# Kernel optimization log

Hardware: AMD Instinct MI355X
Metric: run time of the kernel (lower is better)

Reference implementation:

```python
import jax, jax.numpy as jnp
import numpy as np

B, S, E, H, D = 2, 2048, 1024, 16, 64  # batch, seq(=max_seq_len), embed_dim, heads, atten_dim


def setup_inputs() -> dict:
    key = jax.random.key(0)
    ks = jax.random.split(key, 9)
    s = 0.02
    return {
        "x": jax.random.normal(ks[0], (B, S, E), jnp.float32),
        "Wq": jax.random.normal(ks[1], (H, E, D), jnp.float32) * s,
        "Wk": jax.random.normal(ks[2], (H, E, D), jnp.float32) * s,
        "Wv": jax.random.normal(ks[3], (H, E, D), jnp.float32) * s,
        "bq": jax.random.normal(ks[4], (H, D), jnp.float32) * s,
        "bk": jax.random.normal(ks[5], (H, D), jnp.float32) * s,
        "bv": jax.random.normal(ks[6], (H, D), jnp.float32) * s,
        "Wp": jax.random.normal(ks[7], (H * D, E), jnp.float32) * s,
        "bp": jax.random.normal(ks[8], (E,), jnp.float32) * s,
    }


def reference(x, Wq, Wk, Wv, bq, bk, bv, Wp, bp):
    scale = jnp.sqrt(jnp.float32(D))
    # per-head projections, all heads at once: [B,H,S,D]
    q = jnp.einsum("bse,hed->bhsd", x, Wq) + bq[:, None, :]
    k = jnp.einsum("bse,hed->bhsd", x, Wk) + bk[:, None, :]
    v = jnp.einsum("bse,hed->bhsd", x, Wv) + bv[:, None, :]
    # causal scores [B,H,S,S], additive -inf mask above diagonal (as in the buffer)
    score = jnp.einsum("bhsd,bhtd->bhst", q, k) / scale
    mask = jnp.triu(jnp.full((S, S), -jnp.inf, jnp.float32), k=1)
    score = score + mask
    probs = jax.nn.softmax(score, axis=-1)
    attn = jnp.einsum("bhst,bhtd->bhsd", probs, v)
    # concat heads -> [B,S,H*D], then projection + ReLU
    concat = attn.transpose(0, 2, 1, 3).reshape(B, S, H * D)
    out = jax.nn.relu(concat @ Wp + bp)
    return out
```

## Files before the change

### kernel.cpp

```cpp
#include <hip/hip_runtime.h>

#define S_LEN 2048
#define E_DIM 1024
#define H_NUM 16
#define D_DIM 64

typedef unsigned short u16;
using bf16x8 = __attribute__((ext_vector_type(8))) short;
using f32x4  = __attribute__((ext_vector_type(4))) float;

#define MFMA16(A, B, C) __builtin_amdgcn_mfma_f32_16x16x32_bf16(A, B, C, 0, 0, 0)

__device__ __forceinline__ u16 f2bf(float f) {
    unsigned u = __float_as_uint(f);
    u += 0x7fffu + ((u >> 16) & 1u);
    return (u16)(u >> 16);
}
__device__ __forceinline__ f32x4 fzero4() { f32x4 z; z[0]=0.f; z[1]=0.f; z[2]=0.f; z[3]=0.f; return z; }

__device__ __forceinline__ void gll16(const u16* g, u16* l) {
    __builtin_amdgcn_global_load_lds(
        (const __attribute__((address_space(1))) void*)g,
        (__attribute__((address_space(3))) void*)l, 16, 0, 0);
}

__global__ __launch_bounds__(256) void cvt_bf16(const float* __restrict__ in, u16* __restrict__ outp, int n) {
    int i4 = (blockIdx.x * 256 + threadIdx.x) * 4;
    if (i4 < n) {
        float4 f = *(const float4*)(in + i4);
        unsigned lo = (unsigned)f2bf(f.x) | ((unsigned)f2bf(f.y) << 16);
        unsigned hi = (unsigned)f2bf(f.z) | ((unsigned)f2bf(f.w) << 16);
        uint2 p; p.x = lo; p.y = hi;
        *(uint2*)(outp + i4) = p;
    }
}

__device__ __forceinline__ void cvt_t_tile(const float* __restrict__ bin, u16* __restrict__ bout,
                                           int R, int C, int r0, int c0) {
    __shared__ float t[64][65];
    const int tid = threadIdx.x;
    const int lr = tid >> 2, lc = (tid & 3) * 16;

    const float* src = bin + (size_t)(r0 + lr) * C + c0 + lc;
    #pragma unroll
    for (int j = 0; j < 4; j++) {
        float4 f = *(const float4*)(src + j * 4);
        t[lr][lc + j * 4 + 0] = f.x; t[lr][lc + j * 4 + 1] = f.y;
        t[lr][lc + j * 4 + 2] = f.z; t[lr][lc + j * 4 + 3] = f.w;
    }
    __syncthreads();

    u16* dst = bout + (size_t)(c0 + lr) * R + r0 + lc;
    u16 vals[16];
    #pragma unroll
    for (int i = 0; i < 16; i++) vals[i] = f2bf(t[lc + i][lr]);
    uint4 pa, pb;
    pa.x = vals[0] | (vals[1] << 16);  pa.y = vals[2] | (vals[3] << 16);
    pa.z = vals[4] | (vals[5] << 16);  pa.w = vals[6] | (vals[7] << 16);
    pb.x = vals[8] | (vals[9] << 16);  pb.y = vals[10] | (vals[11] << 16);
    pb.z = vals[12] | (vals[13] << 16); pb.w = vals[14] | (vals[15] << 16);
    *(uint4*)dst = pa;
    *(uint4*)(dst + 8) = pb;
}

__global__ __launch_bounds__(256) void cvt_bf16_t(const float* __restrict__ in, u16* __restrict__ outp,
                                                  int R, int C) {
    const float* bin = in + (size_t)blockIdx.z * R * C;
    u16* bout = outp + (size_t)blockIdx.z * R * C;
    cvt_t_tile(bin, bout, R, C, blockIdx.y * 64, blockIdx.x * 64);
}

__global__ __launch_bounds__(256) void cvt_w3_t(
    const float* __restrict__ Wq, const float* __restrict__ Wk, const float* __restrict__ Wv,
    u16* __restrict__ wqt, u16* __restrict__ wkt, u16* __restrict__ wvt) {
    const int which = blockIdx.z >> 4, bh = blockIdx.z & 15;
    const float* in = (which == 0) ? Wq : (which == 1) ? Wk : Wv;
    u16* outp = (which == 0) ? wqt : (which == 1) ? wkt : wvt;
    const float* bin = in + (size_t)bh * E_DIM * D_DIM;
    u16* bout = outp + (size_t)bh * E_DIM * D_DIM;
    cvt_t_tile(bin, bout, E_DIM, D_DIM, blockIdx.y * 64, 0);
}

__global__ __launch_bounds__(256) void vt_prep(const u16* __restrict__ v, u16* __restrict__ vt) {
    const int st = blockIdx.x;
    const int bhi = blockIdx.y;
    __shared__ u16 t[64 * 72];
    const int tid = threadIdx.x;
    const int wave = tid >> 6, lane = tid & 63;

    const u16* src = v + (size_t)bhi * S_LEN * D_DIM + (size_t)(st * 64 + lane) * D_DIM + wave * 16;
    uint4 a = *(const uint4*)(src);
    uint4 b = *(const uint4*)(src + 8);
    unsigned w[8] = { a.x, a.y, a.z, a.w, b.x, b.y, b.z, b.w };
    #pragma unroll
    for (int j = 0; j < 8; j++) {
        t[(wave * 16 + 2 * j    ) * 72 + lane] = (u16)(w[j] & 0xffffu);
        t[(wave * 16 + 2 * j + 1) * 72 + lane] = (u16)(w[j] >> 16);
    }
    __syncthreads();

    const int dr = tid >> 2, sc = (tid & 3) * 16;
    u16* dst = vt + (size_t)bhi * D_DIM * S_LEN + (size_t)dr * S_LEN + st * 64 + sc;
    *(uint4*)(dst    ) = *(const uint4*)(&t[dr * 72 + sc    ]);
    *(uint4*)(dst + 8) = *(const uint4*)(&t[dr * 72 + sc + 8]);
}

__global__ __launch_bounds__(256) void qkv_gemm(
    const u16* __restrict__ xb, const u16* __restrict__ wcat,
    const float* __restrict__ bq, const float* __restrict__ bk, const float* __restrict__ bv,
    u16* __restrict__ oq, u16* __restrict__ okk, u16* __restrict__ ov)
{
    const int m0 = blockIdx.x * 128;
    const int n0 = blockIdx.y * 128;

    __shared__ u16 As[128 * 32];
    __shared__ u16 Bs[128 * 32];

    const int tid  = threadIdx.x;
    const int wave = tid >> 6, lane = tid & 63, quad = lane >> 4, l16 = lane & 15;
    const int mh = wave >> 1, nh = wave & 1;

    const int lrow = lane >> 2, lcol = (lane & 3) * 8;
    const u16* aBase = xb   + (size_t)(m0 + wave * 32 + lrow) * E_DIM + lcol;
    const u16* bBase = wcat + (size_t)(n0 + wave * 32 + lrow) * E_DIM + lcol;
    u16* aLds0 = &As[(wave * 32     ) * 32];
    u16* aLds1 = &As[(wave * 32 + 16) * 32];
    u16* bLds0 = &Bs[(wave * 32     ) * 32];
    u16* bLds1 = &Bs[(wave * 32 + 16) * 32];

    f32x4 acc[4][4];
    #pragma unroll
    for (int j = 0; j < 4; j++)
        #pragma unroll
        for (int mi = 0; mi < 4; mi++) acc[j][mi] = fzero4();

    for (int k0 = 0; k0 < E_DIM; k0 += 32) {
        __syncthreads();
        gll16(aBase + k0,                 aLds0);
        gll16(aBase + k0 + 16 * E_DIM,    aLds1);
        gll16(bBase + k0,                 bLds0);
        gll16(bBase + k0 + 16 * E_DIM,    bLds1);
        __syncthreads();

        bf16x8 af[4];
        #pragma unroll
        for (int mi = 0; mi < 4; mi++)
            af[mi] = *(const bf16x8*)(&As[(mh * 64 + mi * 16 + l16) * 32 + quad * 8]);
        #pragma unroll
        for (int j = 0; j < 4; j++) {
            bf16x8 bfv = *(const bf16x8*)(&Bs[(nh * 64 + j * 16 + l16) * 32 + quad * 8]);
            #pragma unroll
            for (int mi = 0; mi < 4; mi++)
                acc[j][mi] = MFMA16(af[mi], bfv, acc[j][mi]);
        }
    }

    u16* outp[3] = { oq, okk, ov };
    const float* biasp[3] = { bq, bk, bv };
    #pragma unroll
    for (int j = 0; j < 4; j++) {
        const int n = n0 + nh * 64 + j * 16 + l16;
        const int t = n >> 10, h = (n >> 6) & 15, d = n & 63;
        float bia = biasp[t][h * D_DIM + d];
        const float scl = (t == 0) ? 0.125f : 1.0f;
        u16* dst = outp[t];
        #pragma unroll
        for (int mi = 0; mi < 4; mi++) {
            #pragma unroll
            for (int r = 0; r < 4; r++) {
                int m = m0 + mh * 64 + mi * 16 + quad * 4 + r;
                int b = m >> 11, s = m & 2047;
                dst[((size_t)(b * H_NUM + h) * S_LEN + s) * D_DIM + d] =
                    f2bf((acc[j][mi][r] + bia) * scl);
            }
        }
    }
}

__global__ __launch_bounds__(256) void attn_fwd(
    const u16* __restrict__ q, const u16* __restrict__ k, const u16* __restrict__ vt,
    u16* __restrict__ concat)
{
    const int p  = blockIdx.x;
    const int qa = p, qb = 31 - p;
    const int h  = blockIdx.y;
    const int bb = blockIdx.z;

    const size_t headoff = (size_t)(bb * H_NUM + h) * S_LEN * D_DIM;
    const u16* qh  = q  + headoff;
    const u16* kh  = k  + headoff;
    const u16* vth = vt + headoff;

    __shared__ u16 Qa[64 * 72];
    __shared__ u16 Qb[64 * 72];
    __shared__ u16 Ks[64 * 72];
    __shared__ u16 Vts[64 * 72];
    __shared__ u16 Ps[4][16 * 72];

    const int tid  = threadIdx.x;
    const int wave = tid >> 6, lane = tid & 63, quad = lane >> 4, l16 = lane & 15;

    const int srow = tid >> 2, scg = tid & 3;

    {
        const u16* qsa = qh + (size_t)(qa * 64 + srow) * D_DIM + scg * 16;
        const u16* qsb = qh + (size_t)(qb * 64 + srow) * D_DIM + scg * 16;
        *(uint4*)(&Qa[srow * 72 + scg * 16    ]) = *(const uint4*)(qsa);
        *(uint4*)(&Qa[srow * 72 + scg * 16 + 8]) = *(const uint4*)(qsa + 8);
        *(uint4*)(&Qb[srow * 72 + scg * 16    ]) = *(const uint4*)(qsb);
        *(uint4*)(&Qb[srow * 72 + scg * 16 + 8]) = *(const uint4*)(qsb + 8);
    }
    __syncthreads();

    bf16x8 bqa0 = *(const bf16x8*)(&Qa[(wave * 16 + l16) * 72 + quad * 8]);
    bf16x8 bqa1 = *(const bf16x8*)(&Qa[(wave * 16 + l16) * 72 + 32 + quad * 8]);
    bf16x8 bqb0 = *(const bf16x8*)(&Qb[(wave * 16 + l16) * 72 + quad * 8]);
    bf16x8 bqb1 = *(const bf16x8*)(&Qb[(wave * 16 + l16) * 72 + 32 + quad * 8]);

    f32x4 oa[4], ob[4];
    #pragma unroll
    for (int nt = 0; nt < 4; nt++) { oa[nt] = fzero4(); ob[nt] = fzero4(); }
    float la = 0.f, lb = 0.f;

    uint4 kA, kB, vA, vB;
    {
        const u16* ksrc = kh + (size_t)srow * D_DIM + scg * 16;
        kA = *(const uint4*)(ksrc); kB = *(const uint4*)(ksrc + 8);
        const u16* vsrc = vth + (size_t)srow * S_LEN + scg * 16;
        vA = *(const uint4*)(vsrc); vB = *(const uint4*)(vsrc + 8);
    }

    const int qga = qa * 64 + wave * 16 + l16;
    const int qgb = qb * 64 + wave * 16 + l16;

    for (int kt = 0; kt <= qb; kt++) {
        __syncthreads();
        *(uint4*)(&Ks[srow * 72 + scg * 16    ]) = kA;
        *(uint4*)(&Ks[srow * 72 + scg * 16 + 8]) = kB;
        *(uint4*)(&Vts[srow * 72 + scg * 16    ]) = vA;
        *(uint4*)(&Vts[srow * 72 + scg * 16 + 8]) = vB;
        __syncthreads();

        if (kt < qb) {
            const u16* ksrc = kh + (size_t)((kt + 1) * 64 + srow) * D_DIM + scg * 16;
            kA = *(const uint4*)(ksrc); kB = *(const uint4*)(ksrc + 8);
            const u16* vsrc = vth + (size_t)srow * S_LEN + (kt + 1) * 64 + scg * 16;
            vA = *(const uint4*)(vsrc); vB = *(const uint4*)(vsrc + 8);
        }

        const bool both = (kt <= qa);

        f32x4 stb[4], sta[4];
        #pragma unroll
        for (int nt = 0; nt < 4; nt++) {
            bf16x8 ak0 = *(const bf16x8*)(&Ks[(nt * 16 + l16) * 72 + quad * 8]);
            bf16x8 ak1 = *(const bf16x8*)(&Ks[(nt * 16 + l16) * 72 + 32 + quad * 8]);
            stb[nt] = fzero4();
            stb[nt] = MFMA16(ak0, bqb0, stb[nt]);
            stb[nt] = MFMA16(ak1, bqb1, stb[nt]);
            if (both) {
                sta[nt] = fzero4();
                sta[nt] = MFMA16(ak0, bqa0, sta[nt]);
                sta[nt] = MFMA16(ak1, bqa1, sta[nt]);
            }
        }

        {
            u16* pw = &Ps[wave][0];
            #pragma unroll
            for (int nt = 0; nt < 4; nt++) {
                float pe[4];
                if (kt == qb) {
                    #pragma unroll
                    for (int r = 0; r < 4; r++) {
                        int kkg = kt * 64 + nt * 16 + quad * 4 + r;
                        pe[r] = (kkg > qgb) ? 0.f : __expf(stb[nt][r]);
                    }
                } else {
                    #pragma unroll
                    for (int r = 0; r < 4; r++) pe[r] = __expf(stb[nt][r]);
                }
                lb += pe[0] + pe[1] + pe[2] + pe[3];
                uint2 pk;
                pk.x = (unsigned)f2bf(pe[0]) | ((unsigned)f2bf(pe[1]) << 16);
                pk.y = (unsigned)f2bf(pe[2]) | ((unsigned)f2bf(pe[3]) << 16);
                *(uint2*)(&pw[l16 * 72 + nt * 16 + quad * 4]) = pk;
            }
            bf16x8 ap0 = *(const bf16x8*)(&Ps[wave][l16 * 72 + quad * 8]);
            bf16x8 ap1 = *(const bf16x8*)(&Ps[wave][l16 * 72 + 32 + quad * 8]);
            #pragma unroll
            for (int nt = 0; nt < 4; nt++) {
                bf16x8 bv0 = *(const bf16x8*)(&Vts[(nt * 16 + l16) * 72 + quad * 8]);
                bf16x8 bv1 = *(const bf16x8*)(&Vts[(nt * 16 + l16) * 72 + 32 + quad * 8]);
                ob[nt] = MFMA16(ap0, bv0, ob[nt]);
                ob[nt] = MFMA16(ap1, bv1, ob[nt]);
            }
        }

        if (both) {
            u16* pw = &Ps[wave][0];
            #pragma unroll
            for (int nt = 0; nt < 4; nt++) {
                float pe[4];
                if (kt == qa) {
                    #pragma unroll
                    for (int r = 0; r < 4; r++) {
                        int kkg = kt * 64 + nt * 16 + quad * 4 + r;
                        pe[r] = (kkg > qga) ? 0.f : __expf(sta[nt][r]);
                    }
                } else {
                    #pragma unroll
                    for (int r = 0; r < 4; r++) pe[r] = __expf(sta[nt][r]);
                }
                la += pe[0] + pe[1] + pe[2] + pe[3];
                uint2 pk;
                pk.x = (unsigned)f2bf(pe[0]) | ((unsigned)f2bf(pe[1]) << 16);
                pk.y = (unsigned)f2bf(pe[2]) | ((unsigned)f2bf(pe[3]) << 16);
                *(uint2*)(&pw[l16 * 72 + nt * 16 + quad * 4]) = pk;
            }
            bf16x8 ap0 = *(const bf16x8*)(&Ps[wave][l16 * 72 + quad * 8]);
            bf16x8 ap1 = *(const bf16x8*)(&Ps[wave][l16 * 72 + 32 + quad * 8]);
            #pragma unroll
            for (int nt = 0; nt < 4; nt++) {
                bf16x8 bv0 = *(const bf16x8*)(&Vts[(nt * 16 + l16) * 72 + quad * 8]);
                bf16x8 bv1 = *(const bf16x8*)(&Vts[(nt * 16 + l16) * 72 + 32 + quad * 8]);
                oa[nt] = MFMA16(ap0, bv0, oa[nt]);
                oa[nt] = MFMA16(ap1, bv1, oa[nt]);
            }
        }
    }

    lb += __shfl_xor(lb, 16); lb += __shfl_xor(lb, 32);
    la += __shfl_xor(la, 16); la += __shfl_xor(la, 32);

    #pragma unroll
    for (int r = 0; r < 4; r++) {
        const int srcl = quad * 4 + r;
        float lbr = __shfl(lb, srcl);
        float lar = __shfl(la, srcl);
        int sqa = qa * 64 + wave * 16 + quad * 4 + r;
        int sqb = qb * 64 + wave * 16 + quad * 4 + r;
        #pragma unroll
        for (int nt = 0; nt < 4; nt++) {
            concat[((size_t)(bb * S_LEN + sqa)) * E_DIM + h * D_DIM + nt * 16 + l16] =
                f2bf(oa[nt][r] / lar);
            concat[((size_t)(bb * S_LEN + sqb)) * E_DIM + h * D_DIM + nt * 16 + l16] =
                f2bf(ob[nt][r] / lbr);
        }
    }
}

__global__ __launch_bounds__(256) void out_proj(
    const u16* __restrict__ concat, const u16* __restrict__ wpt,
    const float* __restrict__ bp, float* __restrict__ out)
{
    const int m0 = blockIdx.x * 128;
    const int n0 = blockIdx.y * 128;

    __shared__ u16 As[128 * 40];
    __shared__ u16 Bs[128 * 40];

    const int tid  = threadIdx.x;
    const int wave = tid >> 6, lane = tid & 63, quad = lane >> 4, l16 = lane & 15;
    const int mh = wave >> 1, nh = wave & 1;

    const int arow = tid >> 1, acol = (tid & 1) * 16;

    const u16* aptr = concat + (size_t)(m0 + arow) * E_DIM + acol;
    const u16* bptr = wpt + (size_t)(n0 + arow) * E_DIM + acol;

    f32x4 acc[4][4];
    #pragma unroll
    for (int j = 0; j < 4; j++)
        #pragma unroll
        for (int mi = 0; mi < 4; mi++) acc[j][mi] = fzero4();

    uint4 pA0, pA1, pB0, pB1;
    pA0 = *(const uint4*)(aptr);     pA1 = *(const uint4*)(aptr + 8);
    pB0 = *(const uint4*)(bptr);     pB1 = *(const uint4*)(bptr + 8);

    for (int k0 = 0; k0 < E_DIM; k0 += 32) {
        __syncthreads();
        *(uint4*)(&As[arow * 40 + acol    ]) = pA0;
        *(uint4*)(&As[arow * 40 + acol + 8]) = pA1;
        *(uint4*)(&Bs[arow * 40 + acol    ]) = pB0;
        *(uint4*)(&Bs[arow * 40 + acol + 8]) = pB1;
        __syncthreads();

        if (k0 + 32 < E_DIM) {
            pA0 = *(const uint4*)(aptr + k0 + 32);  pA1 = *(const uint4*)(aptr + k0 + 40);
            pB0 = *(const uint4*)(bptr + k0 + 32);  pB1 = *(const uint4*)(bptr + k0 + 40);
        }

        bf16x8 af[4];
        #pragma unroll
        for (int mi = 0; mi < 4; mi++)
            af[mi] = *(const bf16x8*)(&As[(mh * 64 + mi * 16 + l16) * 40 + quad * 8]);
        #pragma unroll
        for (int j = 0; j < 4; j++) {
            bf16x8 bfv = *(const bf16x8*)(&Bs[(nh * 64 + j * 16 + l16) * 40 + quad * 8]);
            #pragma unroll
            for (int mi = 0; mi < 4; mi++)
                acc[j][mi] = MFMA16(af[mi], bfv, acc[j][mi]);
        }
    }

    #pragma unroll
    for (int j = 0; j < 4; j++) {
        int n = n0 + nh * 64 + j * 16 + l16;
        float bia = bp[n];
        #pragma unroll
        for (int mi = 0; mi < 4; mi++) {
            #pragma unroll
            for (int r = 0; r < 4; r++) {
                int m = m0 + mh * 64 + mi * 16 + quad * 4 + r;
                out[(size_t)m * E_DIM + n] = fmaxf(acc[j][mi][r] + bia, 0.f);
            }
        }
    }
}

extern "C" void kernel_launch(void* const* d_in, const int* in_sizes, int n_in,
                              void* d_out, int out_size, void* d_ws, size_t ws_size,
                              hipStream_t stream)
{
    (void)in_sizes; (void)n_in; (void)out_size; (void)ws_size;
    const float* x  = (const float*)d_in[0];
    const float* Wq = (const float*)d_in[1];
    const float* Wk = (const float*)d_in[2];
    const float* Wv = (const float*)d_in[3];
    const float* bq = (const float*)d_in[4];
    const float* bk = (const float*)d_in[5];
    const float* bv = (const float*)d_in[6];
    const float* Wp = (const float*)d_in[7];
    const float* bp = (const float*)d_in[8];
    float* out = (float*)d_out;

    const size_t QKV_ELEMS = (size_t)2 * H_NUM * S_LEN * D_DIM;
    const size_t W_ELEMS   = (size_t)H_NUM * E_DIM * D_DIM;

    u16* q   = (u16*)d_ws;
    u16* k   = q   + QKV_ELEMS;
    u16* v   = k   + QKV_ELEMS;
    u16* cc  = v   + QKV_ELEMS;
    u16* xb  = cc  + QKV_ELEMS;
    u16* wqt = xb  + QKV_ELEMS;
    u16* wkt = wqt + W_ELEMS;
    u16* wvt = wkt + W_ELEMS;
    u16* wpt = wvt + W_ELEMS;
    u16* vtr = xb;

    cvt_bf16<<<dim3(4096), 256, 0, stream>>>(x, xb, (int)QKV_ELEMS);
    cvt_w3_t<<<dim3(1, 16, 48), 256, 0, stream>>>(Wq, Wk, Wv, wqt, wkt, wvt);
    cvt_bf16_t<<<dim3(16, 16, 1), 256, 0, stream>>>(Wp, wpt, H_NUM * D_DIM, E_DIM);

    qkv_gemm<<<dim3(32, 24), 256, 0, stream>>>(xb, wqt, bq, bk, bv, q, k, v);
    vt_prep<<<dim3(32, 32), 256, 0, stream>>>(v, vtr);
    attn_fwd<<<dim3(16, 16, 2), 256, 0, stream>>>(q, k, vtr, cc);
    out_proj<<<dim3(32, 8), 256, 0, stream>>>(cc, wpt, bp, out);
}
```

Before: 199.0 us.

## Write V transposed from QKV GEMM, double-buffer attention K/V via async LDS loads

The QKV GEMM epilogue now writes V directly in transposed [d][s] layout with packed bf16 converts, so the separate vt_prep kernel and its extra pass over V are gone. The attention kernel stages Q, K and V tiles with global_load_lds into XOR-swizzled unpadded LDS. K/V are double-buffered so the next tile's load overlaps compute, which drops one barrier per iteration. The softmax folds log2(e) into the Q scale and uses hardware exp2, packed bf16 conversion and a reciprocal instead of division. The V fragments are loaded once and reused by both query tiles. In exchange it uses more LDS per block and slightly changes rounding.

```diff
diff --git a/kernel.cpp b/kernel.cpp
--- a/kernel.cpp
+++ b/kernel.cpp
@@ -10,6 +10,7 @@
 using f32x4  = __attribute__((ext_vector_type(4))) float;
 
 #define MFMA16(A, B, C) __builtin_amdgcn_mfma_f32_16x16x32_bf16(A, B, C, 0, 0, 0)
+#define QSCALE 0.18033688011112042f
 
 __device__ __forceinline__ u16 f2bf(float f) {
     unsigned u = __float_as_uint(f);
@@ -18,10 +19,44 @@
 }
 __device__ __forceinline__ f32x4 fzero4() { f32x4 z; z[0]=0.f; z[1]=0.f; z[2]=0.f; z[3]=0.f; return z; }
 
+__device__ __forceinline__ unsigned cvtpk(float a, float b) {
+    unsigned r;
+    asm("v_cvt_pk_bf16_f32 %0, %1, %2" : "=v"(r) : "v"(a), "v"(b));
+    return r;
+}
+__device__ __forceinline__ float fexp2(float x) {
+#if __has_builtin(__builtin_amdgcn_exp2f)
+    return __builtin_amdgcn_exp2f(x);
+#else
+    float r; asm("v_exp_f32 %0, %1" : "=v"(r) : "v"(x)); return r;
+#endif
+}
+__device__ __forceinline__ float frcp(float x) {
+#if __has_builtin(__builtin_amdgcn_rcpf)
+    return __builtin_amdgcn_rcpf(x);
+#else
+    float r; asm("v_rcp_f32 %0, %1" : "=v"(r) : "v"(x)); return r;
+#endif
+}
+
 __device__ __forceinline__ void gll16(const u16* g, u16* l) {
     __builtin_amdgcn_global_load_lds(
         (const __attribute__((address_space(1))) void*)g,
         (__attribute__((address_space(3))) void*)l, 16, 0, 0);
+}
+
+__device__ __forceinline__ void stage64(const u16* __restrict__ g, int gstride,
+                                        u16* l, int wave, int lane) {
+    #pragma unroll
+    for (int i = 0; i < 2; i++) {
+        const int r  = wave * 16 + i * 8 + (lane >> 3);
+        const int sl = (lane & 7) ^ (r & 7);
+        gll16(g + (size_t)r * gstride + sl * 8, l + (wave * 16 + i * 8) * 64);
+    }
+}
+__device__ __forceinline__ bf16x8 ldswz(const u16* t, int rr, int hh, int quad) {
+    const int sl = ((hh << 2) + quad) ^ (rr & 7);
+    return *(const bf16x8*)(t + rr * 64 + sl * 8);
 }
 
 __global__ __launch_bounds__(256) void cvt_bf16(const float* __restrict__ in, u16* __restrict__ outp, int n) {
@@ -81,30 +116,6 @@
     cvt_t_tile(bin, bout, E_DIM, D_DIM, blockIdx.y * 64, 0);
 }
 
-__global__ __launch_bounds__(256) void vt_prep(const u16* __restrict__ v, u16* __restrict__ vt) {
-    const int st = blockIdx.x;
-    const int bhi = blockIdx.y;
-    __shared__ u16 t[64 * 72];
-    const int tid = threadIdx.x;
-    const int wave = tid >> 6, lane = tid & 63;
-
-    const u16* src = v + (size_t)bhi * S_LEN * D_DIM + (size_t)(st * 64 + lane) * D_DIM + wave * 16;
-    uint4 a = *(const uint4*)(src);
-    uint4 b = *(const uint4*)(src + 8);
-    unsigned w[8] = { a.x, a.y, a.z, a.w, b.x, b.y, b.z, b.w };
-    #pragma unroll
-    for (int j = 0; j < 8; j++) {
-        t[(wave * 16 + 2 * j    ) * 72 + lane] = (u16)(w[j] & 0xffffu);
-        t[(wave * 16 + 2 * j + 1) * 72 + lane] = (u16)(w[j] >> 16);
-    }
-    __syncthreads();
-
-    const int dr = tid >> 2, sc = (tid & 3) * 16;
-    u16* dst = vt + (size_t)bhi * D_DIM * S_LEN + (size_t)dr * S_LEN + st * 64 + sc;
-    *(uint4*)(dst    ) = *(const uint4*)(&t[dr * 72 + sc    ]);
-    *(uint4*)(dst + 8) = *(const uint4*)(&t[dr * 72 + sc + 8]);
-}
-
 __global__ __launch_bounds__(256) void qkv_gemm(
     const u16* __restrict__ xb, const u16* __restrict__ wcat,
     const float* __restrict__ bq, const float* __restrict__ bk, const float* __restrict__ bv,
@@ -155,23 +166,41 @@
         }
     }
 
-    u16* outp[3] = { oq, okk, ov };
-    const float* biasp[3] = { bq, bk, bv };
-    #pragma unroll
-    for (int j = 0; j < 4; j++) {
-        const int n = n0 + nh * 64 + j * 16 + l16;
-        const int t = n >> 10, h = (n >> 6) & 15, d = n & 63;
-        float bia = biasp[t][h * D_DIM + d];
-        const float scl = (t == 0) ? 0.125f : 1.0f;
-        u16* dst = outp[t];
-        #pragma unroll
-        for (int mi = 0; mi < 4; mi++) {
-            #pragma unroll
-            for (int r = 0; r < 4; r++) {
-                int m = m0 + mh * 64 + mi * 16 + quad * 4 + r;
+    const int t = n0 >> 10;
+    if (t < 2) {
+        const float scl = (t == 0) ? QSCALE : 1.0f;
+        const float* bias = (t == 0) ? bq : bk;
+        u16* dst = (t == 0) ? oq : okk;
+        #pragma unroll
+        for (int j = 0; j < 4; j++) {
+            const int n = n0 + nh * 64 + j * 16 + l16;
+            const int h = (n >> 6) & 15, d = n & 63;
+            float bia = bias[h * D_DIM + d];
+            #pragma unroll
+            for (int mi = 0; mi < 4; mi++) {
+                #pragma unroll
+                for (int r = 0; r < 4; r++) {
+                    int m = m0 + mh * 64 + mi * 16 + quad * 4 + r;
+                    int b = m >> 11, s = m & 2047;
+                    dst[((size_t)(b * H_NUM + h) * S_LEN + s) * D_DIM + d] =
+                        f2bf((acc[j][mi][r] + bia) * scl);
+                }
+            }
+        }
+    } else {
+        #pragma unroll
+        for (int j = 0; j < 4; j++) {
+            const int n = n0 + nh * 64 + j * 16 + l16;
+            const int h = (n >> 6) & 15, d = n & 63;
+            float bia = bv[h * D_DIM + d];
+            #pragma unroll
+            for (int mi = 0; mi < 4; mi++) {
+                int m = m0 + mh * 64 + mi * 16 + quad * 4;
                 int b = m >> 11, s = m & 2047;
-                dst[((size_t)(b * H_NUM + h) * S_LEN + s) * D_DIM + d] =
-                    f2bf((acc[j][mi][r] + bia) * scl);
+                uint2 pk;
+                pk.x = cvtpk(acc[j][mi][0] + bia, acc[j][mi][1] + bia);
+                pk.y = cvtpk(acc[j][mi][2] + bia, acc[j][mi][3] + bia);
+                *(uint2*)(&ov[((size_t)(b * H_NUM + h) * D_DIM + d) * S_LEN + s]) = pk;
             }
         }
     }
@@ -191,79 +220,59 @@
     const u16* kh  = k  + headoff;
     const u16* vth = vt + headoff;
 
-    __shared__ u16 Qa[64 * 72];
-    __shared__ u16 Qb[64 * 72];
-    __shared__ u16 Ks[64 * 72];
-    __shared__ u16 Vts[64 * 72];
+    __shared__ u16 QaL[64 * 64];
+    __shared__ u16 QbL[64 * 64];
+    __shared__ u16 Ks[2][64 * 64];
+    __shared__ u16 Vts[2][64 * 64];
     __shared__ u16 Ps[4][16 * 72];
 
     const int tid  = threadIdx.x;
     const int wave = tid >> 6, lane = tid & 63, quad = lane >> 4, l16 = lane & 15;
 
-    const int srow = tid >> 2, scg = tid & 3;
-
-    {
-        const u16* qsa = qh + (size_t)(qa * 64 + srow) * D_DIM + scg * 16;
-        const u16* qsb = qh + (size_t)(qb * 64 + srow) * D_DIM + scg * 16;
-        *(uint4*)(&Qa[srow * 72 + scg * 16    ]) = *(const uint4*)(qsa);
-        *(uint4*)(&Qa[srow * 72 + scg * 16 + 8]) = *(const uint4*)(qsa + 8);
-        *(uint4*)(&Qb[srow * 72 + scg * 16    ]) = *(const uint4*)(qsb);
-        *(uint4*)(&Qb[srow * 72 + scg * 16 + 8]) = *(const uint4*)(qsb + 8);
-    }
+    stage64(qh + (size_t)qa * 64 * D_DIM, D_DIM, QaL,    wave, lane);
+    stage64(qh + (size_t)qb * 64 * D_DIM, D_DIM, QbL,    wave, lane);
+    stage64(kh,                           D_DIM, Ks[0],  wave, lane);
+    stage64(vth,                          S_LEN, Vts[0], wave, lane);
     __syncthreads();
 
-    bf16x8 bqa0 = *(const bf16x8*)(&Qa[(wave * 16 + l16) * 72 + quad * 8]);
-    bf16x8 bqa1 = *(const bf16x8*)(&Qa[(wave * 16 + l16) * 72 + 32 + quad * 8]);
-    bf16x8 bqb0 = *(const bf16x8*)(&Qb[(wave * 16 + l16) * 72 + quad * 8]);
-    bf16x8 bqb1 = *(const bf16x8*)(&Qb[(wave * 16 + l16) * 72 + 32 + quad * 8]);
+    bf16x8 bqa0 = ldswz(QaL, wave * 16 + l16, 0, quad);
+    bf16x8 bqa1 = ldswz(QaL, wave * 16 + l16, 1, quad);
+    bf16x8 bqb0 = ldswz(QbL, wave * 16 + l16, 0, quad);
+    bf16x8 bqb1 = ldswz(QbL, wave * 16 + l16, 1, quad);
 
     f32x4 oa[4], ob[4];
     #pragma unroll
     for (int nt = 0; nt < 4; nt++) { oa[nt] = fzero4(); ob[nt] = fzero4(); }
     float la = 0.f, lb = 0.f;
 
-    uint4 kA, kB, vA, vB;
-    {
-        const u16* ksrc = kh + (size_t)srow * D_DIM + scg * 16;
-        kA = *(const uint4*)(ksrc); kB = *(const uint4*)(ksrc + 8);
-        const u16* vsrc = vth + (size_t)srow * S_LEN + scg * 16;
-        vA = *(const uint4*)(vsrc); vB = *(const uint4*)(vsrc + 8);
-    }
-
     const int qga = qa * 64 + wave * 16 + l16;
     const int qgb = qb * 64 + wave * 16 + l16;
 
     for (int kt = 0; kt <= qb; kt++) {
-        __syncthreads();
-        *(uint4*)(&Ks[srow * 72 + scg * 16    ]) = kA;
-        *(uint4*)(&Ks[srow * 72 + scg * 16 + 8]) = kB;
-        *(uint4*)(&Vts[srow * 72 + scg * 16    ]) = vA;
-        *(uint4*)(&Vts[srow * 72 + scg * 16 + 8]) = vB;
-        __syncthreads();
-
+        if (kt) __syncthreads();
         if (kt < qb) {
-            const u16* ksrc = kh + (size_t)((kt + 1) * 64 + srow) * D_DIM + scg * 16;
-            kA = *(const uint4*)(ksrc); kB = *(const uint4*)(ksrc + 8);
-            const u16* vsrc = vth + (size_t)srow * S_LEN + (kt + 1) * 64 + scg * 16;
-            vA = *(const uint4*)(vsrc); vB = *(const uint4*)(vsrc + 8);
-        }
-
+            stage64(kh + (size_t)(kt + 1) * 64 * D_DIM, D_DIM, Ks[(kt + 1) & 1],  wave, lane);
+            stage64(vth + (kt + 1) * 64,                S_LEN, Vts[(kt + 1) & 1], wave, lane);
+        }
+        const u16* Kc = Ks[kt & 1];
+        const u16* Vc = Vts[kt & 1];
         const bool both = (kt <= qa);
 
         f32x4 stb[4], sta[4];
         #pragma unroll
         for (int nt = 0; nt < 4; nt++) {
-            bf16x8 ak0 = *(const bf16x8*)(&Ks[(nt * 16 + l16) * 72 + quad * 8]);
-            bf16x8 ak1 = *(const bf16x8*)(&Ks[(nt * 16 + l16) * 72 + 32 + quad * 8]);
-            stb[nt] = fzero4();
-            stb[nt] = MFMA16(ak0, bqb0, stb[nt]);
+            const int rr = nt * 16 + l16;
+            bf16x8 ak0 = ldswz(Kc, rr, 0, quad);
+            bf16x8 ak1 = ldswz(Kc, rr, 1, quad);
+            stb[nt] = MFMA16(ak0, bqb0, fzero4());
             stb[nt] = MFMA16(ak1, bqb1, stb[nt]);
             if (both) {
-                sta[nt] = fzero4();
-                sta[nt] = MFMA16(ak0, bqa0, sta[nt]);
+                sta[nt] = MFMA16(ak0, bqa0, fzero4());
                 sta[nt] = MFMA16(ak1, bqa1, sta[nt]);
             }
         }
+
+        bf16x8 bv0[4], bv1[4];
 
         {
             u16* pw = &Ps[wave][0];
@@ -274,26 +283,26 @@
                     #pragma unroll
                     for (int r = 0; r < 4; r++) {
                         int kkg = kt * 64 + nt * 16 + quad * 4 + r;
-                        pe[r] = (kkg > qgb) ? 0.f : __expf(stb[nt][r]);
+                        pe[r] = (kkg > qgb) ? 0.f : fexp2(stb[nt][r]);
                     }
                 } else {
                     #pragma unroll
-                    for (int r = 0; r < 4; r++) pe[r] = __expf(stb[nt][r]);
+                    for (int r = 0; r < 4; r++) pe[r] = fexp2(stb[nt][r]);
                 }
-                lb += pe[0] + pe[1] + pe[2] + pe[3];
+                lb += (pe[0] + pe[1]) + (pe[2] + pe[3]);
                 uint2 pk;
-                pk.x = (unsigned)f2bf(pe[0]) | ((unsigned)f2bf(pe[1]) << 16);
-                pk.y = (unsigned)f2bf(pe[2]) | ((unsigned)f2bf(pe[3]) << 16);
+                pk.x = cvtpk(pe[0], pe[1]);
+                pk.y = cvtpk(pe[2], pe[3]);
                 *(uint2*)(&pw[l16 * 72 + nt * 16 + quad * 4]) = pk;
             }
             bf16x8 ap0 = *(const bf16x8*)(&Ps[wave][l16 * 72 + quad * 8]);
             bf16x8 ap1 = *(const bf16x8*)(&Ps[wave][l16 * 72 + 32 + quad * 8]);
             #pragma unroll
             for (int nt = 0; nt < 4; nt++) {
-                bf16x8 bv0 = *(const bf16x8*)(&Vts[(nt * 16 + l16) * 72 + quad * 8]);
-                bf16x8 bv1 = *(const bf16x8*)(&Vts[(nt * 16 + l16) * 72 + 32 + quad * 8]);
-                ob[nt] = MFMA16(ap0, bv0, ob[nt]);
-                ob[nt] = MFMA16(ap1, bv1, ob[nt]);
+                bv0[nt] = ldswz(Vc, nt * 16 + l16, 0, quad);
+                bv1[nt] = ldswz(Vc, nt * 16 + l16, 1, quad);
+                ob[nt] = MFMA16(ap0, bv0[nt], ob[nt]);
+                ob[nt] = MFMA16(ap1, bv1[nt], ob[nt]);
             }
         }
 
@@ -306,26 +315,24 @@
                     #pragma unroll
                     for (int r = 0; r < 4; r++) {
                         int kkg = kt * 64 + nt * 16 + quad * 4 + r;
-                        pe[r] = (kkg > qga) ? 0.f : __expf(sta[nt][r]);
+                        pe[r] = (kkg > qga) ? 0.f : fexp2(sta[nt][r]);
                     }
                 } else {
                     #pragma unroll
-                    for (int r = 0; r < 4; r++) pe[r] = __expf(sta[nt][r]);
+                    for (int r = 0; r < 4; r++) pe[r] = fexp2(sta[nt][r]);
                 }
-                la += pe[0] + pe[1] + pe[2] + pe[3];
+                la += (pe[0] + pe[1]) + (pe[2] + pe[3]);
                 uint2 pk;
-                pk.x = (unsigned)f2bf(pe[0]) | ((unsigned)f2bf(pe[1]) << 16);
-                pk.y = (unsigned)f2bf(pe[2]) | ((unsigned)f2bf(pe[3]) << 16);
+                pk.x = cvtpk(pe[0], pe[1]);
+                pk.y = cvtpk(pe[2], pe[3]);
                 *(uint2*)(&pw[l16 * 72 + nt * 16 + quad * 4]) = pk;
             }
             bf16x8 ap0 = *(const bf16x8*)(&Ps[wave][l16 * 72 + quad * 8]);
             bf16x8 ap1 = *(const bf16x8*)(&Ps[wave][l16 * 72 + 32 + quad * 8]);
             #pragma unroll
             for (int nt = 0; nt < 4; nt++) {
-                bf16x8 bv0 = *(const bf16x8*)(&Vts[(nt * 16 + l16) * 72 + quad * 8]);
-                bf16x8 bv1 = *(const bf16x8*)(&Vts[(nt * 16 + l16) * 72 + 32 + quad * 8]);
-                oa[nt] = MFMA16(ap0, bv0, oa[nt]);
-                oa[nt] = MFMA16(ap1, bv1, oa[nt]);
+                oa[nt] = MFMA16(ap0, bv0[nt], oa[nt]);
+                oa[nt] = MFMA16(ap1, bv1[nt], oa[nt]);
             }
         }
     }
@@ -336,16 +343,16 @@
     #pragma unroll
     for (int r = 0; r < 4; r++) {
         const int srcl = quad * 4 + r;
-        float lbr = __shfl(lb, srcl);
-        float lar = __shfl(la, srcl);
+        float lbi = frcp(__shfl(lb, srcl));
+        float lai = frcp(__shfl(la, srcl));
         int sqa = qa * 64 + wave * 16 + quad * 4 + r;
         int sqb = qb * 64 + wave * 16 + quad * 4 + r;
         #pragma unroll
         for (int nt = 0; nt < 4; nt++) {
             concat[((size_t)(bb * S_LEN + sqa)) * E_DIM + h * D_DIM + nt * 16 + l16] =
-                f2bf(oa[nt][r] / lar);
+                f2bf(oa[nt][r] * lai);
             concat[((size_t)(bb * S_LEN + sqb)) * E_DIM + h * D_DIM + nt * 16 + l16] =
-                f2bf(ob[nt][r] / lbr);
+                f2bf(ob[nt][r] * lbi);
         }
     }
 }
@@ -448,14 +455,12 @@
     u16* wkt = wqt + W_ELEMS;
     u16* wvt = wkt + W_ELEMS;
     u16* wpt = wvt + W_ELEMS;
-    u16* vtr = xb;
 
     cvt_bf16<<<dim3(4096), 256, 0, stream>>>(x, xb, (int)QKV_ELEMS);
     cvt_w3_t<<<dim3(1, 16, 48), 256, 0, stream>>>(Wq, Wk, Wv, wqt, wkt, wvt);
     cvt_bf16_t<<<dim3(16, 16, 1), 256, 0, stream>>>(Wp, wpt, H_NUM * D_DIM, E_DIM);
 
     qkv_gemm<<<dim3(32, 24), 256, 0, stream>>>(xb, wqt, bq, bk, bv, q, k, v);
-    vt_prep<<<dim3(32, 32), 256, 0, stream>>>(v, vtr);
-    attn_fwd<<<dim3(16, 16, 2), 256, 0, stream>>>(q, k, vtr, cc);
+    attn_fwd<<<dim3(16, 16, 2), 256, 0, stream>>>(q, k, v, cc);
     out_proj<<<dim3(32, 8), 256, 0, stream>>>(cc, wpt, bp, out);
 }
```

New measurement: 207.1 us. 4.1% more time.
